# Performance work log

Hardware: AMD Instinct MI355X
Metric: run time of the kernel (lower is better)

## Reference

```python
import jax, jax.numpy as jnp
import numpy as np

N_HEAD, D_MODEL, D_VOCAB = 8, 512, 32000
B, P = 8, 512


def setup_inputs() -> dict:
    key = jax.random.key(0)
    k_x, k_w, k_b = jax.random.split(key, 3)
    input_tensor = jax.random.normal(k_x, (B, P, N_HEAD, D_MODEL), dtype=jnp.float32)
    # per-head Linear params, torch layout: weight [d_vocab, d_model], bias [d_vocab]
    bound = 1.0 / np.sqrt(D_MODEL)
    weights = jax.random.uniform(k_w, (N_HEAD, D_VOCAB, D_MODEL), minval=-bound, maxval=bound, dtype=jnp.float32)
    biases = jax.random.uniform(k_b, (N_HEAD, D_VOCAB), minval=-bound, maxval=bound, dtype=jnp.float32)
    return {"input_tensor": input_tensor, "weights": weights, "biases": biases}


def reference(input_tensor, weights, biases) -> jnp.ndarray:
    # sum_h (x[:,:,h,:] @ W_h^T + b_h)  -> single contraction over (h, d)
    # input_tensor: [B, P, H, D]; weights: [H, V, D]; biases: [H, V]
    out = jnp.einsum("bphd,hvd->bpv", input_tensor, weights)
    out = out + biases.sum(axis=0)  # [V] broadcast over [B, P, V]
    return out
```

## Files before the change

kernel.cpp:

```cpp
#include <hip/hip_runtime.h>
#include <hip/hip_bf16.h>
#include <stdint.h>

#define NHEAD 8
#define DMODEL 512
#define DVOCAB 32000
#define M_DIM 4096
#define K_DIM 4096
#define N_DIM 32000
#define NT    64

typedef short bf16x8 __attribute__((ext_vector_type(8)));
typedef float f32x4 __attribute__((ext_vector_type(4)));
typedef unsigned short ushort8 __attribute__((ext_vector_type(8)));

template <int V> struct IC { static constexpr int v = V; };

__device__ __forceinline__ unsigned short f2bf(float f) {
    unsigned int u = __builtin_bit_cast(unsigned int, f);
    u = (u + 0x7fffu + ((u >> 16) & 1u)) >> 16;
    return (unsigned short)u;
}

__device__ __forceinline__ void load16_to_lds(const void* g, void* l) {
    __builtin_amdgcn_global_load_lds(
        (const __attribute__((address_space(1))) unsigned int*)g,
        (__attribute__((address_space(3))) unsigned int*)l, 16, 0, 0);
}

__global__ void cvt_x(const float* __restrict__ in, unsigned short* __restrict__ out) {
    long t = (long)blockIdx.x * 256 + threadIdx.x;
    const float4* s = (const float4*)in + t * 2;
    float4 a = s[0], b = s[1];
    ushort8 o;
    o[0] = f2bf(a.x); o[1] = f2bf(a.y); o[2] = f2bf(a.z); o[3] = f2bf(a.w);
    o[4] = f2bf(b.x); o[5] = f2bf(b.y); o[6] = f2bf(b.z); o[7] = f2bf(b.w);
    *(ushort8*)(out + t * 8) = o;
}

__global__ void cvt_w(const float* __restrict__ in, unsigned short* __restrict__ out) {
    int t = blockIdx.x * 256 + threadIdx.x;
    int d8 = t & 63;
    int hv = t >> 6;
    int h = hv / DVOCAB;
    int v = hv - h * DVOCAB;
    const float4* s = (const float4*)(in + (long)hv * DMODEL + d8 * 8);
    float4 a = s[0], b = s[1];
    ushort8 o;
    o[0] = f2bf(a.x); o[1] = f2bf(a.y); o[2] = f2bf(a.z); o[3] = f2bf(a.w);
    o[4] = f2bf(b.x); o[5] = f2bf(b.y); o[6] = f2bf(b.z); o[7] = f2bf(b.w);
    *(ushort8*)(out + (long)v * K_DIM + h * DMODEL + d8 * 8) = o;
}

__global__ void bias_red(const float* __restrict__ b, float* __restrict__ out) {
    int v = blockIdx.x * 256 + threadIdx.x;
    if (v >= DVOCAB) return;
    float s = 0.f;
    #pragma unroll
    for (int h = 0; h < NHEAD; ++h) s += b[h * DVOCAB + v];
    out[v] = s;
}

#define BAR()    __builtin_amdgcn_s_barrier()
#define VMCNT6() asm volatile("s_waitcnt vmcnt(6)" ::: "memory")
#define VMCNT0() asm volatile("s_waitcnt vmcnt(0)" ::: "memory")

__global__ __launch_bounds__(512, 2) void gemm256(
    const unsigned short* __restrict__ A,
    const unsigned short* __restrict__ B,
    const float* __restrict__ bias,
    float* __restrict__ C)
{
    __shared__ __attribute__((aligned(16))) unsigned short lds[2][2][2][8192];

    const int tid = threadIdx.x;
    const int bid = blockIdx.x;
    const int xcd = bid & 7, j = bid >> 3;
    const int mt = xcd * 2 + (j & 1);
    const int nt = j >> 1;
    const long m0 = (long)mt * 256;
    const long n0 = (long)nt * 256;

    const int wid = tid >> 6, lane = tid & 63;
    const int wr = wid >> 2, wc = wid & 3;
    const int lr = lane & 15, lk = lane >> 4;
    const int swz = lr & 7;

    const unsigned short* pA[2];
    const unsigned short* pB[2];
    #pragma unroll
    for (int ks = 0; ks < 2; ++ks) {
        const int ch = ((ks << 2) | lk) ^ swz;
        pA[ks] = &lds[0][0][0][0] + (wr * 64 + lr) * 64 + ch * 8;
        pB[ks] = &lds[1][0][0][0] + (wc * 32 + lr) * 64 + ch * 8;
    }
    #define LDA(mi, ks, HALF, CURB) \
        (*(const bf16x8*)(pA[ks] + (mi) * 1024 + (HALF) * 16384 + (CURB) * 8192))
    #define LDB(nj, ks, HALF, CURB) \
        (*(const bf16x8*)(pB[ks] + (nj) * 1024 + (HALF) * 16384 + (CURB) * 8192))

    const char* Ab = (const char*)(A + m0 * K_DIM);
    const char* Bb = (const char*)(B + n0 * K_DIM);
    const int row0 = tid >> 3,         c0 = (tid & 7) ^ (row0 & 7);
    const int row1 = (512 + tid) >> 3, c1 = ((512 + tid) & 7) ^ (row1 & 7);
    unsigned int a00 = (unsigned)(row0 * K_DIM + c0 * 8) * 2u;
    unsigned int a01 = (unsigned)(row1 * K_DIM + c1 * 8) * 2u;
    unsigned int a10 = (unsigned)((128 + row0) * K_DIM + c0 * 8) * 2u;
    unsigned int a11 = (unsigned)((128 + row1) * K_DIM + c1 * 8) * 2u;
    unsigned int b00 = a00, b01 = a01, b10 = a10, b11 = a11;

    #define ST_A0(CURB) do { \
        load16_to_lds(Ab + a00, (char*)&lds[0][0][(CURB)][0] + tid * 16); \
        load16_to_lds(Ab + a01, (char*)&lds[0][0][(CURB)][0] + 8192 + tid * 16); \
        a00 += 128; a01 += 128; } while (0)
    #define ST_A1(CURB) do { \
        load16_to_lds(Ab + a10, (char*)&lds[0][1][(CURB)][0] + tid * 16); \
        load16_to_lds(Ab + a11, (char*)&lds[0][1][(CURB)][0] + 8192 + tid * 16); \
        a10 += 128; a11 += 128; } while (0)
    #define ST_B0(CURB) do { \
        load16_to_lds(Bb + b00, (char*)&lds[1][0][(CURB)][0] + tid * 16); \
        load16_to_lds(Bb + b01, (char*)&lds[1][0][(CURB)][0] + 8192 + tid * 16); \
        b00 += 128; b01 += 128; } while (0)
    #define ST_B1(CURB) do { \
        load16_to_lds(Bb + b10, (char*)&lds[1][1][(CURB)][0] + tid * 16); \
        load16_to_lds(Bb + b11, (char*)&lds[1][1][(CURB)][0] + 8192 + tid * 16); \
        b10 += 128; b11 += 128; } while (0)

    #define MFQUAD(AF, BF, MO, NO) do {                                        \
        _Pragma("unroll")                                                      \
        for (int ks = 0; ks < 2; ++ks)                                         \
            _Pragma("unroll")                                                  \
            for (int mi = 0; mi < 4; ++mi)                                     \
                _Pragma("unroll")                                              \
                for (int nj = 0; nj < 2; ++nj)                                 \
                    acc[(MO) + mi][(NO) + nj] =                                \
                        __builtin_amdgcn_mfma_f32_16x16x32_bf16(               \
                            AF[mi][ks], BF[nj][ks], acc[(MO) + mi][(NO) + nj], \
                            0, 0, 0);                                          \
    } while (0)

    f32x4 acc[8][4];
    #pragma unroll
    for (int i = 0; i < 8; ++i)
        #pragma unroll
        for (int jn = 0; jn < 4; ++jn)
            acc[i][jn] = (f32x4){0.f, 0.f, 0.f, 0.f};

    bf16x8 af[4][2], bf0[2][2], bf1[2][2];

    ST_A0(0); ST_B0(0); ST_B1(0); ST_A1(0);
    ST_A0(1); ST_B0(1); ST_B1(1);
    VMCNT6();
    BAR();

    auto body = [&](auto curc, int t) {
        constexpr int CUR = decltype(curc)::v;

        #pragma unroll
        for (int mi = 0; mi < 4; ++mi) {
            af[mi][0] = LDA(mi, 0, 0, CUR);
            af[mi][1] = LDA(mi, 1, 0, CUR);
        }
        #pragma unroll
        for (int nj = 0; nj < 2; ++nj) {
            bf0[nj][0] = LDB(nj, 0, 0, CUR);
            bf0[nj][1] = LDB(nj, 1, 0, CUR);
        }
        if (t + 1 < NT) ST_A1(CUR ^ 1);
        BAR();
        __builtin_amdgcn_s_setprio(1);
        MFQUAD(af, bf0, 0, 0);
        __builtin_amdgcn_s_setprio(0);
        BAR();

        #pragma unroll
        for (int nj = 0; nj < 2; ++nj) {
            bf1[nj][0] = LDB(nj, 0, 1, CUR);
            bf1[nj][1] = LDB(nj, 1, 1, CUR);
        }
        if (t + 2 < NT) ST_A0(CUR);
        BAR();
        __builtin_amdgcn_s_setprio(1);
        MFQUAD(af, bf1, 0, 2);
        __builtin_amdgcn_s_setprio(0);
        BAR();

        #pragma unroll
        for (int mi = 0; mi < 4; ++mi) {
            af[mi][0] = LDA(mi, 0, 1, CUR);
            af[mi][1] = LDA(mi, 1, 1, CUR);
        }
        if (t + 2 < NT) { ST_B0(CUR); ST_B1(CUR); }
        if (t < NT - 2) { VMCNT6(); } else { VMCNT0(); }
        BAR();
        __builtin_amdgcn_s_setprio(1);
        MFQUAD(af, bf0, 4, 0);
        MFQUAD(af, bf1, 4, 2);
        __builtin_amdgcn_s_setprio(0);
        BAR();
    };

    for (int t = 0; t < NT; t += 2) {
        body(IC<0>{}, t);
        body(IC<1>{}, t + 1);
    }
    #undef LDA
    #undef LDB
    #undef ST_A0
    #undef ST_A1
    #undef ST_B0
    #undef ST_B1
    #undef MFQUAD

    #pragma unroll
    for (int nj = 0; nj < 4; ++nj) {
        const long col = n0 + (nj >> 1) * 128 + wc * 32 + (nj & 1) * 16 + lr;
        const float bs = bias[col];
        #pragma unroll
        for (int mi = 0; mi < 8; ++mi) {
            const long row = m0 + (mi >> 2) * 128 + wr * 64 + (mi & 3) * 16 + lk * 4;
            #pragma unroll
            for (int r = 0; r < 4; ++r)
                __builtin_nontemporal_store(acc[mi][nj][r] + bs,
                                            &C[(row + r) * (long)N_DIM + col]);
        }
    }
}

__global__ void naive_out(const float* __restrict__ x, const float* __restrict__ w,
                          const float* __restrict__ b, float* __restrict__ out) {
    long idx = (long)blockIdx.x * 256 + threadIdx.x;
    if (idx >= (long)M_DIM * N_DIM) return;
    long m = idx / N_DIM;
    int v = (int)(idx - m * N_DIM);
    float s = 0.f;
    for (int h = 0; h < NHEAD; ++h) {
        const float* xr = x + m * K_DIM + h * DMODEL;
        const float* wr = w + ((long)h * DVOCAB + v) * DMODEL;
        float ps = 0.f;
        for (int d = 0; d < DMODEL; ++d) ps += xr[d] * wr[d];
        s += ps + b[h * DVOCAB + v];
    }
    out[idx] = s;
}

extern "C" void kernel_launch(void* const* d_in, const int* in_sizes, int n_in,
                              void* d_out, int out_size, void* d_ws, size_t ws_size,
                              hipStream_t stream) {
    const float* x = (const float*)d_in[0];
    const float* w = (const float*)d_in[1];
    const float* b = (const float*)d_in[2];
    float* out = (float*)d_out;

    const size_t xbf_bytes = (size_t)M_DIM * K_DIM * 2;
    const size_t wbf_bytes = (size_t)N_DIM * K_DIM * 2;
    const size_t bs_bytes  = (size_t)N_DIM * 4;
    const size_t need = xbf_bytes + wbf_bytes + bs_bytes;

    if (ws_size < need) {
        long total = (long)M_DIM * N_DIM;
        int blocks = (int)((total + 255) / 256);
        naive_out<<<blocks, 256, 0, stream>>>(x, w, b, out);
        return;
    }

    unsigned short* xbf = (unsigned short*)d_ws;
    unsigned short* wbf = (unsigned short*)((char*)d_ws + xbf_bytes);
    float* bsum = (float*)((char*)d_ws + xbf_bytes + wbf_bytes);

    cvt_x<<<8192, 256, 0, stream>>>(x, xbf);
    cvt_w<<<64000, 256, 0, stream>>>(w, wbf);
    bias_red<<<125, 256, 0, stream>>>(b, bsum);
    gemm256<<<2000, 512, 0, stream>>>(xbf, wbf, bsum, out);
}
```

Baseline: 1.066 ms.

## Preload both A halves and reorder MFMA phases to drop a barrier

The GEMM main loop now reads both halves of the A fragments (afL and afH) from LDS early, together with both B halves, instead of reloading A midway. The MFMA quadrants are reordered and one workgroup barrier per k-step is removed, so LDS reads and global-to-LDS prefetches overlap more with matrix work. Per-stream global address counters are replaced by a single running offset plus constant deltas, which cuts address arithmetic and registers. In exchange, eight extra bf16x8 fragments stay live, which raises VGPR pressure and could affect occupancy or cause spills.

```diff
diff --git a/kernel.cpp b/kernel.cpp
--- a/kernel.cpp
+++ b/kernel.cpp
@@ -103,28 +103,26 @@
     const char* Bb = (const char*)(B + n0 * K_DIM);
     const int row0 = tid >> 3,         c0 = (tid & 7) ^ (row0 & 7);
     const int row1 = (512 + tid) >> 3, c1 = ((512 + tid) & 7) ^ (row1 & 7);
-    unsigned int a00 = (unsigned)(row0 * K_DIM + c0 * 8) * 2u;
-    unsigned int a01 = (unsigned)(row1 * K_DIM + c1 * 8) * 2u;
-    unsigned int a10 = (unsigned)((128 + row0) * K_DIM + c0 * 8) * 2u;
-    unsigned int a11 = (unsigned)((128 + row1) * K_DIM + c1 * 8) * 2u;
-    unsigned int b00 = a00, b01 = a01, b10 = a10, b11 = a11;
+    unsigned int cur0 = (unsigned)(row0 * K_DIM + c0 * 8) * 2u;
+    const unsigned int d01 = (unsigned)((row1 - row0) * K_DIM + (c1 - c0) * 8) * 2u;
 
     #define ST_A0(CURB) do { \
-        load16_to_lds(Ab + a00, (char*)&lds[0][0][(CURB)][0] + tid * 16); \
-        load16_to_lds(Ab + a01, (char*)&lds[0][0][(CURB)][0] + 8192 + tid * 16); \
-        a00 += 128; a01 += 128; } while (0)
+        load16_to_lds(Ab + cur0,       (char*)&lds[0][0][(CURB)][0] + tid * 16); \
+        load16_to_lds(Ab + cur0 + d01, (char*)&lds[0][0][(CURB)][0] + 8192 + tid * 16); \
+    } while (0)
     #define ST_A1(CURB) do { \
-        load16_to_lds(Ab + a10, (char*)&lds[0][1][(CURB)][0] + tid * 16); \
-        load16_to_lds(Ab + a11, (char*)&lds[0][1][(CURB)][0] + 8192 + tid * 16); \
-        a10 += 128; a11 += 128; } while (0)
+        load16_to_lds(Ab + cur0 + 0x100000u,       (char*)&lds[0][1][(CURB)][0] + tid * 16); \
+        load16_to_lds(Ab + cur0 + 0x100000u + d01, (char*)&lds[0][1][(CURB)][0] + 8192 + tid * 16); \
+    } while (0)
     #define ST_B0(CURB) do { \
-        load16_to_lds(Bb + b00, (char*)&lds[1][0][(CURB)][0] + tid * 16); \
-        load16_to_lds(Bb + b01, (char*)&lds[1][0][(CURB)][0] + 8192 + tid * 16); \
-        b00 += 128; b01 += 128; } while (0)
+        load16_to_lds(Bb + cur0,       (char*)&lds[1][0][(CURB)][0] + tid * 16); \
+        load16_to_lds(Bb + cur0 + d01, (char*)&lds[1][0][(CURB)][0] + 8192 + tid * 16); \
+    } while (0)
     #define ST_B1(CURB) do { \
-        load16_to_lds(Bb + b10, (char*)&lds[1][1][(CURB)][0] + tid * 16); \
-        load16_to_lds(Bb + b11, (char*)&lds[1][1][(CURB)][0] + 8192 + tid * 16); \
-        b10 += 128; b11 += 128; } while (0)
+        load16_to_lds(Bb + cur0 + 0x100000u,       (char*)&lds[1][1][(CURB)][0] + tid * 16); \
+        load16_to_lds(Bb + cur0 + 0x100000u + d01, (char*)&lds[1][1][(CURB)][0] + 8192 + tid * 16); \
+    } while (0)
+
 
     #define MFQUAD(AF, BF, MO, NO) do {                                        \
         _Pragma("unroll")                                                      \
@@ -146,9 +144,10 @@
         for (int jn = 0; jn < 4; ++jn)
             acc[i][jn] = (f32x4){0.f, 0.f, 0.f, 0.f};
 
-    bf16x8 af[4][2], bf0[2][2], bf1[2][2];
+    bf16x8 afL[4][2], afH[4][2], bf0[2][2], bf1[2][2];
 
     ST_A0(0); ST_B0(0); ST_B1(0); ST_A1(0);
+    cur0 += 128;
     ST_A0(1); ST_B0(1); ST_B1(1);
     VMCNT6();
     BAR();
@@ -158,44 +157,44 @@
 
         #pragma unroll
         for (int mi = 0; mi < 4; ++mi) {
-            af[mi][0] = LDA(mi, 0, 0, CUR);
-            af[mi][1] = LDA(mi, 1, 0, CUR);
+            afL[mi][0] = LDA(mi, 0, 0, CUR);
+            afL[mi][1] = LDA(mi, 1, 0, CUR);
         }
         #pragma unroll
         for (int nj = 0; nj < 2; ++nj) {
             bf0[nj][0] = LDB(nj, 0, 0, CUR);
             bf0[nj][1] = LDB(nj, 1, 0, CUR);
         }
-        if (t + 1 < NT) ST_A1(CUR ^ 1);
-        BAR();
-        __builtin_amdgcn_s_setprio(1);
-        MFQUAD(af, bf0, 0, 0);
-        __builtin_amdgcn_s_setprio(0);
-        BAR();
-
+        if (t + 1 < NT) { ST_A1(CUR ^ 1); }
+        cur0 += 128;
+        BAR();
         #pragma unroll
         for (int nj = 0; nj < 2; ++nj) {
             bf1[nj][0] = LDB(nj, 0, 1, CUR);
             bf1[nj][1] = LDB(nj, 1, 1, CUR);
         }
+        #pragma unroll
+        for (int mi = 0; mi < 4; ++mi) {
+            afH[mi][0] = LDA(mi, 0, 1, CUR);
+            afH[mi][1] = LDA(mi, 1, 1, CUR);
+        }
+        __builtin_amdgcn_s_setprio(1);
+        MFQUAD(afL, bf0, 0, 0);
+        __builtin_amdgcn_s_setprio(0);
+        BAR();
+
         if (t + 2 < NT) ST_A0(CUR);
-        BAR();
         __builtin_amdgcn_s_setprio(1);
-        MFQUAD(af, bf1, 0, 2);
+        MFQUAD(afH, bf0, 4, 0);
         __builtin_amdgcn_s_setprio(0);
         BAR();
 
-        #pragma unroll
-        for (int mi = 0; mi < 4; ++mi) {
-            af[mi][0] = LDA(mi, 0, 1, CUR);
-            af[mi][1] = LDA(mi, 1, 1, CUR);
-        }
         if (t + 2 < NT) { ST_B0(CUR); ST_B1(CUR); }
         if (t < NT - 2) { VMCNT6(); } else { VMCNT0(); }
         BAR();
         __builtin_amdgcn_s_setprio(1);
-        MFQUAD(af, bf0, 4, 0);
-        MFQUAD(af, bf1, 4, 2);
+        MFQUAD(afL, bf1, 0, 2);
+        MFQUAD(afH, bf1, 4, 2);
         __builtin_amdgcn_s_setprio(0);
         BAR();
     };
```

Result: slower. 1.103 ms (+3.5%).

## Make GEMM persistent over eight M tiles per block, prefetching across tiles

Applied to the files above, without the earlier changes.

The launch drops from 2000 one-tile blocks to 250 blocks. Each block owns one 256-column N tile and walks eight consecutive 256-row M tiles. The load pipeline carries into the next M tile's first K steps, so there is no cold start per tile, and the bias is loaded once per block. The aim is to cut block launch and pipeline-refill overhead and to reuse the same W tile from cache. In exchange only about one block runs per CU instead of two, which halves the waves available to hide latency. Each tile's epilogue stores also now sit serially inside the loop.

```diff
diff --git a/kernel.cpp b/kernel.cpp
--- a/kernel.cpp
+++ b/kernel.cpp
@@ -75,10 +75,8 @@
 
     const int tid = threadIdx.x;
     const int bid = blockIdx.x;
-    const int xcd = bid & 7, j = bid >> 3;
-    const int mt = xcd * 2 + (j & 1);
-    const int nt = j >> 1;
-    const long m0 = (long)mt * 256;
+    const int nt  = bid % 125;
+    const int mh  = bid / 125;
     const long n0 = (long)nt * 256;
 
     const int wid = tid >> 6, lane = tid & 63;
@@ -99,32 +97,31 @@
     #define LDB(nj, ks, HALF, CURB) \
         (*(const bf16x8*)(pB[ks] + (nj) * 1024 + (HALF) * 16384 + (CURB) * 8192))
 
-    const char* Ab = (const char*)(A + m0 * K_DIM);
-    const char* Bb = (const char*)(B + n0 * K_DIM);
     const int row0 = tid >> 3,         c0 = (tid & 7) ^ (row0 & 7);
     const int row1 = (512 + tid) >> 3, c1 = ((512 + tid) & 7) ^ (row1 & 7);
-    unsigned int a00 = (unsigned)(row0 * K_DIM + c0 * 8) * 2u;
-    unsigned int a01 = (unsigned)(row1 * K_DIM + c1 * 8) * 2u;
-    unsigned int a10 = (unsigned)((128 + row0) * K_DIM + c0 * 8) * 2u;
-    unsigned int a11 = (unsigned)((128 + row1) * K_DIM + c1 * 8) * 2u;
-    unsigned int b00 = a00, b01 = a01, b10 = a10, b11 = a11;
-
-    #define ST_A0(CURB) do { \
-        load16_to_lds(Ab + a00, (char*)&lds[0][0][(CURB)][0] + tid * 16); \
-        load16_to_lds(Ab + a01, (char*)&lds[0][0][(CURB)][0] + 8192 + tid * 16); \
-        a00 += 128; a01 += 128; } while (0)
-    #define ST_A1(CURB) do { \
-        load16_to_lds(Ab + a10, (char*)&lds[0][1][(CURB)][0] + tid * 16); \
-        load16_to_lds(Ab + a11, (char*)&lds[0][1][(CURB)][0] + 8192 + tid * 16); \
-        a10 += 128; a11 += 128; } while (0)
-    #define ST_B0(CURB) do { \
-        load16_to_lds(Bb + b00, (char*)&lds[1][0][(CURB)][0] + tid * 16); \
-        load16_to_lds(Bb + b01, (char*)&lds[1][0][(CURB)][0] + 8192 + tid * 16); \
-        b00 += 128; b01 += 128; } while (0)
-    #define ST_B1(CURB) do { \
-        load16_to_lds(Bb + b10, (char*)&lds[1][1][(CURB)][0] + tid * 16); \
-        load16_to_lds(Bb + b11, (char*)&lds[1][1][(CURB)][0] + 8192 + tid * 16); \
-        b10 += 128; b11 += 128; } while (0)
+    const unsigned int lo0 = (unsigned)(row0 * K_DIM + c0 * 8) * 2u;
+    const unsigned int d01 = (unsigned)((row1 - row0) * K_DIM + (c1 - c0) * 8) * 2u;
+
+    const char* Ab_i = (const char*)A + (size_t)mh * 8 * 0x200000u;
+    const char* Ab_n = Ab_i + 0x200000u;
+    const char* Bb   = (const char*)(B + n0 * K_DIM);
+
+    #define ST_A0(CURB, AB, UW) do { \
+        load16_to_lds((AB) + lo0 + ((unsigned)(UW) << 7),       (char*)&lds[0][0][(CURB)][0] + tid * 16); \
+        load16_to_lds((AB) + lo0 + d01 + ((unsigned)(UW) << 7), (char*)&lds[0][0][(CURB)][0] + 8192 + tid * 16); \
+    } while (0)
+    #define ST_A1(CURB, AB, UW) do { \
+        load16_to_lds((AB) + lo0 + 0x100000u + ((unsigned)(UW) << 7),       (char*)&lds[0][1][(CURB)][0] + tid * 16); \
+        load16_to_lds((AB) + lo0 + 0x100000u + d01 + ((unsigned)(UW) << 7), (char*)&lds[0][1][(CURB)][0] + 8192 + tid * 16); \
+    } while (0)
+    #define ST_B0(CURB, UW) do { \
+        load16_to_lds(Bb + lo0 + ((unsigned)(UW) << 7),       (char*)&lds[1][0][(CURB)][0] + tid * 16); \
+        load16_to_lds(Bb + lo0 + d01 + ((unsigned)(UW) << 7), (char*)&lds[1][0][(CURB)][0] + 8192 + tid * 16); \
+    } while (0)
+    #define ST_B1(CURB, UW) do { \
+        load16_to_lds(Bb + lo0 + 0x100000u + ((unsigned)(UW) << 7),       (char*)&lds[1][1][(CURB)][0] + tid * 16); \
+        load16_to_lds(Bb + lo0 + 0x100000u + d01 + ((unsigned)(UW) << 7), (char*)&lds[1][1][(CURB)][0] + 8192 + tid * 16); \
+    } while (0)
 
     #define MFQUAD(AF, BF, MO, NO) do {                                        \
         _Pragma("unroll")                                                      \
@@ -146,15 +143,24 @@
         for (int jn = 0; jn < 4; ++jn)
             acc[i][jn] = (f32x4){0.f, 0.f, 0.f, 0.f};
 
+    float bs[4];
+    #pragma unroll
+    for (int nj = 0; nj < 4; ++nj)
+        bs[nj] = bias[n0 + (nj >> 1) * 128 + wc * 32 + (nj & 1) * 16 + lr];
+
     bf16x8 af[4][2], bf0[2][2], bf1[2][2];
 
-    ST_A0(0); ST_B0(0); ST_B1(0); ST_A1(0);
-    ST_A0(1); ST_B0(1); ST_B1(1);
+    ST_A0(0, Ab_i, 0); ST_B0(0, 0); ST_B1(0, 0); ST_A1(0, Ab_i, 0);
+    ST_A0(1, Ab_i, 1); ST_B0(1, 1); ST_B1(1, 1);
     VMCNT6();
     BAR();
 
-    auto body = [&](auto curc, int t) {
+    auto body = [&](auto curc, int t, bool lastT) {
         constexpr int CUR = decltype(curc)::v;
+        int u1 = t + 1; const char* AS1 = Ab_i; if (u1 >= NT) { u1 -= NT; AS1 = Ab_n; }
+        int u2 = t + 2; const char* AS2 = Ab_i; if (u2 >= NT) { u2 -= NT; AS2 = Ab_n; }
+        const bool st1 = !lastT || (t + 1 < NT);
+        const bool st2 = !lastT || (t + 2 < NT);
 
         #pragma unroll
         for (int mi = 0; mi < 4; ++mi) {
@@ -166,7 +172,7 @@
             bf0[nj][0] = LDB(nj, 0, 0, CUR);
             bf0[nj][1] = LDB(nj, 1, 0, CUR);
         }
-        if (t + 1 < NT) ST_A1(CUR ^ 1);
+        if (st1) ST_A1(CUR ^ 1, AS1, u1);
         BAR();
         __builtin_amdgcn_s_setprio(1);
         MFQUAD(af, bf0, 0, 0);
@@ -178,7 +184,7 @@
             bf1[nj][0] = LDB(nj, 0, 1, CUR);
             bf1[nj][1] = LDB(nj, 1, 1, CUR);
         }
-        if (t + 2 < NT) ST_A0(CUR);
+        if (st2) ST_A0(CUR, AS2, u2);
         BAR();
         __builtin_amdgcn_s_setprio(1);
         MFQUAD(af, bf1, 0, 2);
@@ -190,8 +196,8 @@
             af[mi][0] = LDA(mi, 0, 1, CUR);
             af[mi][1] = LDA(mi, 1, 1, CUR);
         }
-        if (t + 2 < NT) { ST_B0(CUR); ST_B1(CUR); }
-        if (t < NT - 2) { VMCNT6(); } else { VMCNT0(); }
+        if (st2) { ST_B0(CUR, u2); ST_B1(CUR, u2); }
+        if (lastT && t >= NT - 2) { VMCNT0(); } else { VMCNT6(); }
         BAR();
         __builtin_amdgcn_s_setprio(1);
         MFQUAD(af, bf0, 4, 0);
@@ -200,9 +206,27 @@
         BAR();
     };
 
-    for (int t = 0; t < NT; t += 2) {
-        body(IC<0>{}, t);
-        body(IC<1>{}, t + 1);
+    for (int i = 0; i < 8; ++i) {
+        const bool lastT = (i == 7);
+        for (int t = 0; t < NT; t += 2) {
+            body(IC<0>{}, t, lastT);
+            body(IC<1>{}, t + 1, lastT);
+        }
+        const long m0i = (long)(mh * 8 + i) * 256;
+        #pragma unroll
+        for (int nj = 0; nj < 4; ++nj) {
+            const long col = n0 + (nj >> 1) * 128 + wc * 32 + (nj & 1) * 16 + lr;
+            #pragma unroll
+            for (int mi = 0; mi < 8; ++mi) {
+                const long row = m0i + (mi >> 2) * 128 + wr * 64 + (mi & 3) * 16 + lk * 4;
+                #pragma unroll
+                for (int r = 0; r < 4; ++r)
+                    __builtin_nontemporal_store(acc[mi][nj][r] + bs[nj],
+                                                &C[(row + r) * (long)N_DIM + col]);
+                acc[mi][nj] = (f32x4){0.f, 0.f, 0.f, 0.f};
+            }
+        }
+        Ab_i = Ab_n; Ab_n += 0x200000u;
     }
     #undef LDA
     #undef LDB
@@ -211,20 +235,6 @@
     #undef ST_B0
     #undef ST_B1
     #undef MFQUAD
-
-    #pragma unroll
-    for (int nj = 0; nj < 4; ++nj) {
-        const long col = n0 + (nj >> 1) * 128 + wc * 32 + (nj & 1) * 16 + lr;
-        const float bs = bias[col];
-        #pragma unroll
-        for (int mi = 0; mi < 8; ++mi) {
-            const long row = m0 + (mi >> 2) * 128 + wr * 64 + (mi & 3) * 16 + lk * 4;
-            #pragma unroll
-            for (int r = 0; r < 4; ++r)
-                __builtin_nontemporal_store(acc[mi][nj][r] + bs,
-                                            &C[(row + r) * (long)N_DIM + col]);
-        }
-    }
 }
 
 __global__ void naive_out(const float* __restrict__ x, const float* __restrict__ w,
@@ -271,5 +281,5 @@
     cvt_x<<<8192, 256, 0, stream>>>(x, xbf);
     cvt_w<<<64000, 256, 0, stream>>>(w, wbf);
     bias_red<<<125, 256, 0, stream>>>(b, bsum);
-    gemm256<<<2000, 512, 0, stream>>>(xbf, wbf, bsum, out);
-}
+    gemm256<<<250, 512, 0, stream>>>(xbf, wbf, bsum, out);
+}
```

Result: slower. 1.088 ms (+2.1%).
